# Kernel tuning notes

Hardware: AMD Instinct MI355X
Metric: run time of the kernel (lower is better)

## Reference

```python
import jax, jax.numpy as jnp
import numpy as np

FIELDS, NUM, CAT = 39, 13, 26
D, M, V, B, DEEP = 16, 16, 100000, 4096, 400
LEFT, RIGHT = np.triu_indices(FIELDS, k=1)  # pair indices, Q = 741
Q = LEFT.size
EPS = 1e-5


def setup_inputs() -> dict:
    key = jax.random.key(0)
    ks = jax.random.split(key, 18)
    xi = jax.random.randint(ks[0], (B, CAT), 0, V)
    xv = jax.random.uniform(ks[1], (B, NUM), dtype=jnp.float32)
    # 2nd-order embedding tables, stacked since all fields share vocab size
    emb_tables = jax.random.normal(ks[2], (FIELDS, V, D), dtype=jnp.float32) * 0.1
    T3 = jax.random.normal(ks[3], (D, M, D), dtype=jnp.float32) * 0.05
    T2 = jax.random.normal(ks[4], (M, D * D), dtype=jnp.float32) * 0.05
    gc = jax.random.normal(ks[5], (Q,), dtype=jnp.float32)
    fi_w = jax.random.normal(ks[6], (Q * M, DEEP), dtype=jnp.float32) * 0.01
    fi_b = jnp.zeros((DEEP,), dtype=jnp.float32)
    fi_gamma = jnp.ones((DEEP,), dtype=jnp.float32)
    fi_beta = jnp.zeros((DEEP,), dtype=jnp.float32)
    emb_w = jax.random.normal(ks[7], (FIELDS * D, DEEP), dtype=jnp.float32) * 0.02
    emb_b = jnp.zeros((DEEP,), dtype=jnp.float32)
    emb_gamma = jnp.ones((DEEP,), dtype=jnp.float32)
    emb_beta = jnp.zeros((DEEP,), dtype=jnp.float32)
    fc_w = jax.random.normal(ks[8], (2 * DEEP, 1), dtype=jnp.float32) * 0.05
    fc_b = jnp.zeros((1,), dtype=jnp.float32)
    return {"xi": xi, "xv": xv, "emb_tables": emb_tables, "T3": T3, "T2": T2,
            "gc": gc, "fi_w": fi_w, "fi_b": fi_b, "fi_gamma": fi_gamma, "fi_beta": fi_beta,
            "emb_w": emb_w, "emb_b": emb_b, "emb_gamma": emb_gamma, "emb_beta": emb_beta,
            "fc_w": fc_w, "fc_b": fc_b}


def _bn(x, gamma, beta):
    # BatchNorm1d in training mode: batch statistics, biased variance
    mean = jnp.mean(x, axis=0)
    var = jnp.var(x, axis=0)
    return gamma * (x - mean) * jax.lax.rsqrt(var + EPS) + beta


def reference(xi, xv, emb_tables, T3, T2, gc, fi_w, fi_b, fi_gamma, fi_beta,
              emb_w, emb_b, emb_gamma, emb_beta, fc_w, fc_b):
    # numerical fields: embedding row 0 scaled by the raw value
    num_part = xv[:, :, None] * emb_tables[:NUM, 0, :][None]          # [B, 13, D]
    # categorical fields: per-field gather
    cat_part = emb_tables[NUM + jnp.arange(CAT)[None, :], xi]          # [B, 26, D]
    fm2 = jnp.concatenate([num_part, cat_part], axis=1)               # [B, 39, D]
    vi = fm2[:, LEFT]                                                  # [B, Q, D]
    vj = fm2[:, RIGHT]                                                 # [B, Q, D]
    # einsum('bqd,dmd,bqd->bm'): repeated d on T3 takes its diagonal -> [D, M]
    T3diag = jnp.einsum('dmd->dm', T3)
    ga = jnp.einsum('bqd,bqd,dm->bm', vi, vj, T3diag)                  # [B, M]
    ga = jax.nn.softmax(ga, axis=1)
    # T1 = einsum('bm,mn->bmn'); s = einsum('bqd,bmn,bqd->bqm') sums T1 over n
    t1_rowsum = ga * jnp.sum(T2, axis=1)[None, :]                      # [B, M]
    pair_dot = jnp.einsum('bqd,bqd->bq', vi, vj)                       # [B, Q]
    s = pair_dot[:, :, None] * t1_rowsum[:, None, :]                   # [B, Q, M]
    sh = (s * gc[None, :, None]).reshape(-1, Q * M)                    # [B, Q*M]
    th = jax.nn.relu(_bn(sh @ fi_w + fi_b, fi_gamma, fi_beta))         # [B, DEEP]
    emb = fm2.reshape(-1, FIELDS * D)                                  # [B, 39*D]
    emb = jax.nn.relu(_bn(emb @ emb_w + emb_b, emb_gamma, emb_beta))   # [B, DEEP]
    out = jnp.concatenate([th, emb], axis=1) @ fc_w + fc_b             # [B, 1]
    return jnp.sum(jax.nn.sigmoid(out), axis=1)                        # [B]
```

## Files before the change

### kernel.cpp

```cpp
#include <hip/hip_runtime.h>
#include <hip/hip_bf16.h>

#define BATCH 4096
#define FIELDS_ 39
#define NUMF 13
#define CATF 26
#define DD 16
#define MM 16
#define VV 100000
#define DEEP_ 400
#define QQ 741
#define QPAD 768
#define KE 624
#define KEP 640
#define NEP 512
#define N1 6400
#define NKTE 20
#define NT_ 24
#define EPS_ 1e-5f

#define OFF_ABF 0
#define OFF_T   (BATCH*QPAD/2)
#define OFF_W2  (OFF_T + BATCH*MM)
#define OFF_WE  (OFF_W2 + N1*QPAD/2)
#define OFF_FMB (OFF_WE + NEP*KEP/2)
#define OFF_TH  (OFF_FMB + BATCH*KEP/2)
#define OFF_EMB (OFF_TH + BATCH*DEEP_)
#define OFF_ACC (OFF_EMB + BATCH*DEEP_)
#define OFF_T2S (OFF_ACC + 1600)
#define OFF_T3D (OFF_T2S + 16)
#define OFF_QIJ (OFF_T3D + 256)

typedef __attribute__((ext_vector_type(8))) short bf16x8;
typedef __attribute__((ext_vector_type(4))) float f32x4;

__device__ __forceinline__ ushort f2bf(float v) {
    union { float f; unsigned u; } x; x.f = v;
    unsigned r = x.u + 0x7fff + ((x.u >> 16) & 1);
    return (ushort)(r >> 16);
}
__device__ __forceinline__ unsigned pack2(float a, float b) {
    return (unsigned)f2bf(a) | ((unsigned)f2bf(b) << 16);
}
__device__ __forceinline__ void async16(void* lds, const void* g) {
    __builtin_amdgcn_global_load_lds(
        (const __attribute__((address_space(1))) unsigned int*)g,
        (__attribute__((address_space(3))) unsigned int*)lds,
        16, 0, 0);
}

__global__ __launch_bounds__(256) void kprep_all(const float* __restrict__ T3,
                                                 const float* __restrict__ T2,
                                                 const float* __restrict__ fi_w,
                                                 const float* __restrict__ emb_w,
                                                 float* __restrict__ ws,
                                                 ushort* __restrict__ W2,
                                                 ushort* __restrict__ WE) {
    __shared__ float tile[32][401];
    int bid = blockIdx.x, tid = threadIdx.x;
    if (bid == 0) {
        if (tid < MM) {
            float s = 0.f;
            for (int j = 0; j < DD * DD; ++j) s += T2[tid * DD * DD + j];
            ws[OFF_T2S + tid] = s;
        }
        if (tid < DD * MM) {
            int d = tid >> 4, m = tid & 15;
            ws[OFF_T3D + tid] = T3[(d * MM + m) * DD + d];
        }
        for (int i = tid; i < 1600; i += 256) ws[OFF_ACC + i] = 0.f;
        int* qij = (int*)(ws + OFF_QIJ);
        for (int q = tid; q < QPAD; q += 256) {
            int v = 0;
            if (q < QQ) {
                int i = 0, qq = q, cnt = FIELDS_ - 1;
                while (qq >= cnt) { qq -= cnt; ++i; cnt = FIELDS_ - 1 - i; }
                v = (i << 8) | (i + 1 + qq);
            }
            qij[q] = v;
        }
    } else if (bid <= 384) {
        int kt = (bid - 1) >> 4, m = (bid - 1) & 15;
        for (int i = tid; i < 32 * 100; i += 256) {
            int ql = i / 100, c4 = i - ql * 100;
            int q = kt * 32 + ql;
            float4 v = make_float4(0.f, 0.f, 0.f, 0.f);
            if (q < QQ) v = *(const float4*)&fi_w[(q * MM + m) * DEEP_ + c4 * 4];
            tile[ql][c4 * 4 + 0] = v.x; tile[ql][c4 * 4 + 1] = v.y;
            tile[ql][c4 * 4 + 2] = v.z; tile[ql][c4 * 4 + 3] = v.w;
        }
        __syncthreads();
        for (int i = tid; i < 400 * 4; i += 256) {
            int kcol = i >> 2, cq = i & 3;
            unsigned r[4];
#pragma unroll
            for (int j = 0; j < 4; ++j)
                r[j] = pack2(tile[cq * 8 + 2 * j][kcol], tile[cq * 8 + 2 * j + 1][kcol]);
            *(uint4*)&W2[(long)(kcol * 16 + m) * QPAD + kt * 32 + cq * 8] =
                make_uint4(r[0], r[1], r[2], r[3]);
        }
    } else {
        int kt = bid - 385;
        for (int i = tid; i < 32 * 100; i += 256) {
            int kl = i / 100, c4 = i - kl * 100;
            int k = kt * 32 + kl;
            float4 v = make_float4(0.f, 0.f, 0.f, 0.f);
            if (k < KE) v = *(const float4*)&emb_w[k * DEEP_ + c4 * 4];
            tile[kl][c4 * 4 + 0] = v.x; tile[kl][c4 * 4 + 1] = v.y;
            tile[kl][c4 * 4 + 2] = v.z; tile[kl][c4 * 4 + 3] = v.w;
        }
        __syncthreads();
        for (int i = tid; i < 512 * 4; i += 256) {
            int n = i >> 2, cq = i & 3;
            uint4 o = make_uint4(0, 0, 0, 0);
            if (n < DEEP_) {
                unsigned r[4];
#pragma unroll
                for (int j = 0; j < 4; ++j)
                    r[j] = pack2(tile[cq * 8 + 2 * j][n], tile[cq * 8 + 2 * j + 1][n]);
                o = make_uint4(r[0], r[1], r[2], r[3]);
            }
            *(uint4*)&WE[(long)n * KEP + kt * 32 + cq * 8] = o;
        }
    }
}

__global__ __launch_bounds__(256) void kfeat(const int* __restrict__ xi,
                                             const float* __restrict__ xv,
                                             const float* __restrict__ emb,
                                             const float* __restrict__ gc,
                                             float* __restrict__ ws,
                                             ushort* __restrict__ Abf,
                                             ushort* __restrict__ FMB) {
    __shared__ float row[KE];
    __shared__ float hsh[DD];
    __shared__ float gash[MM];
    int b = blockIdx.x, tid = threadIdx.x;
    for (int e = tid; e < KE; e += 256) {
        int f = e >> 4, d = e & 15;
        float v;
        if (f < NUMF) {
            v = xv[b * NUMF + f] * emb[(long)f * VV * DD + d];
        } else {
            int c = f - NUMF;
            int idxv = xi[b * CATF + c];
            v = emb[((long)(NUMF + c) * VV + idxv) * DD + d];
        }
        row[e] = v;
    }
    __syncthreads();
    for (int e = tid; e < KEP; e += 256)
        FMB[(long)b * KEP + e] = (e < KE) ? f2bf(row[e]) : (ushort)0;
    if (tid < DD) {
        float s = 0.f, s2 = 0.f;
        for (int f = 0; f < FIELDS_; ++f) { float v = row[f * DD + tid]; s += v; s2 += v * v; }
        hsh[tid] = 0.5f * (s * s - s2);
    }
    __syncthreads();
    if (tid < MM) {
        float g = 0.f;
        for (int d = 0; d < DD; ++d) g += hsh[d] * ws[OFF_T3D + d * MM + tid];
        gash[tid] = g;
    }
    __syncthreads();
    if (tid < MM) {
        float mx = -1e30f;
        for (int m = 0; m < MM; ++m) mx = fmaxf(mx, gash[m]);
        float se = 0.f;
        for (int m = 0; m < MM; ++m) se += expf(gash[m] - mx);
        ws[OFF_T + b * MM + tid] = expf(gash[tid] - mx) / se * ws[OFF_T2S + tid];
    }
    const int* qij = (const int*)(ws + OFF_QIJ);
    for (int q = tid; q < QPAD; q += 256) {
        float av = 0.f;
        if (q < QQ) {
            int ij = qij[q];
            int i = ij >> 8, j = ij & 255;
            float dot = 0.f;
#pragma unroll
            for (int d = 0; d < DD; ++d) dot += row[i * DD + d] * row[j * DD + d];
            av = dot * gc[q];
        }
        Abf[(long)b * QPAD + q] = f2bf(av);
    }
}

__device__ __forceinline__ void pipeline(const ushort* As, const ushort* Bs0,
                                         const ushort* Bs1, ushort* lds0, ushort* lds1,
                                         int tid, int nt, int f1b, int f2b, int sw,
                                         f32x4 (*acc)[4]) {
#define STAGEP(L, T) { \
    async16((L) + tid * 8, As + (T) * 32); \
    async16((L) + 4096 + tid * 8, Bs0 + (T) * 32); \
    async16((L) + 8192 + tid * 8, Bs1 + (T) * 32); }
    STAGEP(lds0, 0);
    asm volatile("s_waitcnt vmcnt(0)" ::: "memory");
    __builtin_amdgcn_s_barrier();
    for (int t = 0; t < nt; ++t) {
        __builtin_amdgcn_sched_barrier(0);
        ushort* cur = (t & 1) ? lds1 : lds0;
        ushort* nxt = (t & 1) ? lds0 : lds1;
        bf16x8 f1[4], f2[4];
#pragma unroll
        for (int r = 0; r < 4; ++r) f1[r] = *(const bf16x8*)&cur[f1b + r * 512 + sw];
#pragma unroll
        for (int c = 0; c < 4; ++c) f2[c] = *(const bf16x8*)&cur[f2b + c * 512 + sw];
        if (t + 1 < nt) STAGEP(nxt, t + 1);
        __builtin_amdgcn_s_setprio(1);
#pragma unroll
        for (int r = 0; r < 4; ++r)
#pragma unroll
            for (int c = 0; c < 4; ++c)
                acc[r][c] = __builtin_amdgcn_mfma_f32_16x16x32_bf16(f1[r], f2[c], acc[r][c], 0, 0, 0);
        __builtin_amdgcn_s_setprio(0);
        if (t + 1 < nt) { asm volatile("s_waitcnt vmcnt(0)" ::: "memory"); }
        __builtin_amdgcn_s_barrier();
    }
#undef STAGEP
}

__global__ __launch_bounds__(512, 4) void kgemms(const ushort* __restrict__ Abf,
                                                 const ushort* __restrict__ W2,
                                                 const ushort* __restrict__ FMB,
                                                 const ushort* __restrict__ WE,
                                                 const float* __restrict__ Tmat,
                                                 float* __restrict__ TH,
                                                 float* __restrict__ EMB,
                                                 float* __restrict__ ACC) {
    __shared__ ushort lds0[12288];
    __shared__ ushort lds1[12288];
    __shared__ float red[512];
    int tid = threadIdx.x;
    int lane = tid & 63, wid = tid >> 6;
    int wb = wid >> 2, wn = wid & 3;
    int kq = lane >> 4, lr = lane & 15;
    int arow = tid >> 2, ac = tid & 3;
    int csw = (ac ^ ((arow >> 1) & 3)) * 8;
    int sw = (kq ^ ((lr >> 1) & 3)) * 8;
    red[tid < 512 ? tid : 0] = 0.f;
    f32x4 acc[4][4] = {};
    int wg = blockIdx.x;

    if (wg < 800) {
        int s = (wg & 7) * 100 + (wg >> 3);
        int n0 = (s >> 5) * 256, b0 = (s & 31) * 128;
        const ushort* As  = Abf + (long)(b0 + arow) * QPAD + csw;
        const ushort* Bs0 = W2 + (long)(n0 + arow) * QPAD + csw;
        const ushort* Bs1 = W2 + (long)(n0 + 128 + arow) * QPAD + csw;
        pipeline(As, Bs0, Bs1, lds0, lds1, tid, NT_,
                 4096 + (wn * 64 + lr) * 32, (wb * 64 + lr) * 32, sw, acc);
        float ls[4] = {0.f, 0.f, 0.f, 0.f}, ls2[4] = {0.f, 0.f, 0.f, 0.f};
#pragma unroll
        for (int cg = 0; cg < 4; ++cg) {
            int bloc = wb * 64 + cg * 16 + lr;
            float4 t4 = *(const float4*)&Tmat[(b0 + bloc) * 16 + kq * 4];
#pragma unroll
            for (int r = 0; r < 4; ++r) {
                float v = acc[r][cg][0] * t4.x + acc[r][cg][1] * t4.y +
                          acc[r][cg][2] * t4.z + acc[r][cg][3] * t4.w;
                v += __shfl_xor(v, 16);
                v += __shfl_xor(v, 32);
                ls[r] += v; ls2[r] += v * v;
                if (lane < 16)
                    TH[(b0 + bloc) * DEEP_ + (n0 >> 4) + wn * 4 + r] = v;
            }
        }
#pragma unroll
        for (int r = 0; r < 4; ++r) {
            float a = ls[r], b2 = ls2[r];
            a += __shfl_xor(a, 8, 16); b2 += __shfl_xor(b2, 8, 16);
            a += __shfl_xor(a, 4, 16); b2 += __shfl_xor(b2, 4, 16);
            a += __shfl_xor(a, 2, 16); b2 += __shfl_xor(b2, 2, 16);
            a += __shfl_xor(a, 1, 16); b2 += __shfl_xor(b2, 1, 16);
            if (lane == 0) {
                atomicAdd(&red[wn * 4 + r], a);
                atomicAdd(&red[16 + wn * 4 + r], b2);
            }
        }
        __syncthreads();
        if (tid < 16) {
            atomicAdd(&ACC[(n0 >> 4) + tid], red[tid]);
            atomicAdd(&ACC[800 + (n0 >> 4) + tid], red[16 + tid]);
        }
    } else {
        int e = wg - 800;
        int se = (e & 7) * 8 + (e >> 3);
        int n0 = (se >> 5) * 256, b0 = (se & 31) * 128;
        const ushort* As  = FMB + (long)(b0 + arow) * KEP + csw;
        const ushort* Bs0 = WE + (long)(n0 + arow) * KEP + csw;
        const ushort* Bs1 = WE + (long)(n0 + 128 + arow) * KEP + csw;
        pipeline(As, Bs0, Bs1, lds0, lds1, tid, NKTE,
                 (wb * 64 + lr) * 32, 4096 + (wn * 64 + lr) * 32, sw, acc);
#pragma unroll
        for (int cg = 0; cg < 4; ++cg) {
            int ncl = wn * 64 + cg * 16 + lr;
            int nc = n0 + ncl;
            float ls = 0.f, ls2 = 0.f;
#pragma unroll
            for (int r = 0; r < 4; ++r) {
#pragma unroll
                for (int j = 0; j < 4; ++j) {
                    float v = acc[r][cg][j];
                    int brow = b0 + wb * 64 + r * 16 + kq * 4 + j;
                    if (nc < DEEP_) EMB[brow * DEEP_ + nc] = v;
                    ls += v; ls2 += v * v;
                }
            }
            ls += __shfl_xor(ls, 16);  ls += __shfl_xor(ls, 32);
            ls2 += __shfl_xor(ls2, 16); ls2 += __shfl_xor(ls2, 32);
            if (lane < 16 && nc < DEEP_) {
                atomicAdd(&red[ncl], ls);
                atomicAdd(&red[256 + ncl], ls2);
            }
        }
        __syncthreads();
        if (tid < 256) {
            int nc = n0 + tid;
            if (nc < DEEP_) {
                atomicAdd(&ACC[400 + nc], red[tid]);
                atomicAdd(&ACC[1200 + nc], red[256 + tid]);
            }
        }
    }
}

__global__ __launch_bounds__(256) void kfinal(const float* fig, const float* fibeta,
                                              const float* eg, const float* ebeta,
                                              const float* fcw, const float* fcb,
                                              const float* ws, float* out) {
    int b = blockIdx.x, tid = threadIdx.x;
    float part = 0.f;
    for (int c = tid; c < 800; c += 256) {
        float x, g, be;
        if (c < DEEP_) { x = ws[OFF_TH + b * DEEP_ + c]; g = fig[c]; be = fibeta[c]; }
        else { int cc = c - DEEP_; x = ws[OFF_EMB + b * DEEP_ + cc]; g = eg[cc]; be = ebeta[cc]; }
        float sm = ws[OFF_ACC + c], sq = ws[OFF_ACC + 800 + c];
        float mean = sm * (1.f / BATCH);
        float var = sq * (1.f / BATCH) - mean * mean;
        float rstd = rsqrtf(var + EPS_);
        float v = fmaxf(g * (x - mean) * rstd + be, 0.f);
        part += v * fcw[c];
    }
    __shared__ float red[4];
#pragma unroll
    for (int off = 32; off > 0; off >>= 1) part += __shfl_down(part, off, 64);
    if ((tid & 63) == 0) red[tid >> 6] = part;
    __syncthreads();
    if (tid == 0) {
        float tot = red[0] + red[1] + red[2] + red[3] + fcb[0];
        out[b] = 1.f / (1.f + expf(-tot));
    }
}

extern "C" void kernel_launch(void* const* d_in, const int* in_sizes, int n_in,
                              void* d_out, int out_size, void* d_ws, size_t ws_size,
                              hipStream_t stream) {
    const int*   xi    = (const int*)d_in[0];
    const float* xv    = (const float*)d_in[1];
    const float* emb   = (const float*)d_in[2];
    const float* T3    = (const float*)d_in[3];
    const float* T2    = (const float*)d_in[4];
    const float* gc    = (const float*)d_in[5];
    const float* fi_w  = (const float*)d_in[6];
    const float* fig   = (const float*)d_in[8];
    const float* fibt  = (const float*)d_in[9];
    const float* emb_w = (const float*)d_in[10];
    const float* eg    = (const float*)d_in[12];
    const float* ebt   = (const float*)d_in[13];
    const float* fcw   = (const float*)d_in[14];
    const float* fcb   = (const float*)d_in[15];
    float* ws = (float*)d_ws;
    ushort* Abf = (ushort*)(ws + OFF_ABF);
    ushort* W2  = (ushort*)(ws + OFF_W2);
    ushort* WE  = (ushort*)(ws + OFF_WE);
    ushort* FMB = (ushort*)(ws + OFF_FMB);
    float* out = (float*)d_out;

    hipLaunchKernelGGL(kprep_all, dim3(405), dim3(256), 0, stream,
                       T3, T2, fi_w, emb_w, ws, W2, WE);
    hipLaunchKernelGGL(kfeat, dim3(BATCH), dim3(256), 0, stream, xi, xv, emb, gc, ws, Abf, FMB);
    hipLaunchKernelGGL(kgemms, dim3(864), dim3(512), 0, stream,
                       Abf, W2, FMB, WE, ws + OFF_T, ws + OFF_TH, ws + OFF_EMB, ws + OFF_ACC);
    hipLaunchKernelGGL(kfinal, dim3(BATCH), dim3(256), 0, stream,
                       fig, fibt, eg, ebt, fcw, fcb, ws, out);
}
```

Before: 92.58 us.

## Fuse feature and weight-prep kernels, triple-buffer GEMM pipeline, vectorize stores

Splits the weight transpose/bf16 conversion into finer blocks and merges it with the per-sample feature kernel into one launch, so the two independent jobs overlap. The feature path now stages its bf16 outputs in shared memory and writes them with wide stores. It also computes the pair indices inline instead of reading a precomputed table. The GEMM pipeline goes from double to triple buffering with a prefetch distance of two and skips the final barrier. TH results are staged in LDS for float4 stores, and kfinal uses float4 loads. The triple buffer raises LDS use per block, which may reduce occupancy.

```diff
diff --git a/kernel.cpp b/kernel.cpp
--- a/kernel.cpp
+++ b/kernel.cpp
@@ -29,7 +29,6 @@
 #define OFF_ACC (OFF_EMB + BATCH*DEEP_)
 #define OFF_T2S (OFF_ACC + 1600)
 #define OFF_T3D (OFF_T2S + 16)
-#define OFF_QIJ (OFF_T3D + 256)
 
 typedef __attribute__((ext_vector_type(8))) short bf16x8;
 typedef __attribute__((ext_vector_type(4))) float f32x4;
@@ -49,163 +48,172 @@
         16, 0, 0);
 }
 
-__global__ __launch_bounds__(256) void kprep_all(const float* __restrict__ T3,
-                                                 const float* __restrict__ T2,
-                                                 const float* __restrict__ fi_w,
-                                                 const float* __restrict__ emb_w,
-                                                 float* __restrict__ ws,
-                                                 ushort* __restrict__ W2,
-                                                 ushort* __restrict__ WE) {
-    __shared__ float tile[32][401];
+__global__ __launch_bounds__(256) void kprep0(const float* __restrict__ T3,
+                                              const float* __restrict__ T2,
+                                              float* __restrict__ ws) {
+    int tid = threadIdx.x;
+    if (tid < MM) {
+        float s = 0.f;
+        for (int j = 0; j < DD * DD; ++j) s += T2[tid * DD * DD + j];
+        ws[OFF_T2S + tid] = s;
+    }
+    if (tid < DD * MM) {
+        int d = tid >> 4, m = tid & 15;
+        ws[OFF_T3D + tid] = T3[(d * MM + m) * DD + d];
+    }
+    for (int i = tid; i < 1600; i += 256) ws[OFF_ACC + i] = 0.f;
+}
+
+__global__ __launch_bounds__(256) void kbig(const int* __restrict__ xi,
+                                            const float* __restrict__ xv,
+                                            const float* __restrict__ emb,
+                                            const float* __restrict__ gc,
+                                            const float* __restrict__ fi_w,
+                                            const float* __restrict__ emb_w,
+                                            float* __restrict__ ws,
+                                            ushort* __restrict__ Abf,
+                                            ushort* __restrict__ FMB,
+                                            ushort* __restrict__ W2,
+                                            ushort* __restrict__ WE) {
+    __shared__ float smem[4200];
     int bid = blockIdx.x, tid = threadIdx.x;
-    if (bid == 0) {
+
+    if (bid < BATCH) {
+        float* row = smem;
+        float* hsh = smem + 624;
+        float* gash = smem + 640;
+        ushort* stA = (ushort*)(smem + 656);
+        ushort* stF = stA + QPAD;
+        int b = bid;
+        for (int e = tid; e < KE; e += 256) {
+            int f = e >> 4, d = e & 15;
+            float v;
+            if (f < NUMF) {
+                v = xv[b * NUMF + f] * emb[(long)f * VV * DD + d];
+            } else {
+                int c = f - NUMF;
+                int idxv = xi[b * CATF + c];
+                v = emb[((long)(NUMF + c) * VV + idxv) * DD + d];
+            }
+            row[e] = v;
+        }
+        __syncthreads();
+        for (int e = tid; e < KEP; e += 256)
+            stF[e] = (e < KE) ? f2bf(row[e]) : (ushort)0;
+        if (tid < DD) {
+            float s = 0.f, s2 = 0.f;
+            for (int f = 0; f < FIELDS_; ++f) { float v = row[f * DD + tid]; s += v; s2 += v * v; }
+            hsh[tid] = 0.5f * (s * s - s2);
+        }
+        __syncthreads();
         if (tid < MM) {
-            float s = 0.f;
-            for (int j = 0; j < DD * DD; ++j) s += T2[tid * DD * DD + j];
-            ws[OFF_T2S + tid] = s;
-        }
-        if (tid < DD * MM) {
-            int d = tid >> 4, m = tid & 15;
-            ws[OFF_T3D + tid] = T3[(d * MM + m) * DD + d];
-        }
-        for (int i = tid; i < 1600; i += 256) ws[OFF_ACC + i] = 0.f;
-        int* qij = (int*)(ws + OFF_QIJ);
+            float g = 0.f;
+            for (int d = 0; d < DD; ++d) g += hsh[d] * ws[OFF_T3D + d * MM + tid];
+            gash[tid] = g;
+        }
+        __syncthreads();
+        if (tid < MM) {
+            float mx = -1e30f;
+            for (int m = 0; m < MM; ++m) mx = fmaxf(mx, gash[m]);
+            float se = 0.f;
+            for (int m = 0; m < MM; ++m) se += expf(gash[m] - mx);
+            ws[OFF_T + b * MM + tid] = expf(gash[tid] - mx) / se * ws[OFF_T2S + tid];
+        }
         for (int q = tid; q < QPAD; q += 256) {
-            int v = 0;
+            float av = 0.f;
             if (q < QQ) {
                 int i = 0, qq = q, cnt = FIELDS_ - 1;
                 while (qq >= cnt) { qq -= cnt; ++i; cnt = FIELDS_ - 1 - i; }
-                v = (i << 8) | (i + 1 + qq);
-            }
-            qij[q] = v;
-        }
-    } else if (bid <= 384) {
-        int kt = (bid - 1) >> 4, m = (bid - 1) & 15;
-        for (int i = tid; i < 32 * 100; i += 256) {
-            int ql = i / 100, c4 = i - ql * 100;
+                int j = i + 1 + qq;
+                float dot = 0.f;
+#pragma unroll
+                for (int d = 0; d < DD; ++d) dot += row[i * DD + d] * row[j * DD + d];
+                av = dot * gc[q];
+            }
+            stA[q] = f2bf(av);
+        }
+        __syncthreads();
+        if (tid < 96)
+            *(uint4*)&Abf[(long)b * QPAD + tid * 8] = *(uint4*)&stA[tid * 8];
+        else if (tid < 176)
+            *(uint4*)&FMB[(long)b * KEP + (tid - 96) * 8] = *(uint4*)&stF[(tid - 96) * 8];
+    } else if (bid < BATCH + 1536) {
+        int bt = bid - BATCH;
+        int kt = bt >> 6, m = (bt >> 2) & 15, ch = bt & 3;
+        float* tile = smem;
+        for (int i = tid; i < 32 * 25; i += 256) {
+            int ql = i / 25, c4 = i - ql * 25;
             int q = kt * 32 + ql;
             float4 v = make_float4(0.f, 0.f, 0.f, 0.f);
-            if (q < QQ) v = *(const float4*)&fi_w[(q * MM + m) * DEEP_ + c4 * 4];
-            tile[ql][c4 * 4 + 0] = v.x; tile[ql][c4 * 4 + 1] = v.y;
-            tile[ql][c4 * 4 + 2] = v.z; tile[ql][c4 * 4 + 3] = v.w;
-        }
-        __syncthreads();
-        for (int i = tid; i < 400 * 4; i += 256) {
-            int kcol = i >> 2, cq = i & 3;
+            if (q < QQ) v = *(const float4*)&fi_w[(q * MM + m) * DEEP_ + ch * 100 + c4 * 4];
+            tile[ql * 101 + c4 * 4 + 0] = v.x; tile[ql * 101 + c4 * 4 + 1] = v.y;
+            tile[ql * 101 + c4 * 4 + 2] = v.z; tile[ql * 101 + c4 * 4 + 3] = v.w;
+        }
+        __syncthreads();
+        for (int i = tid; i < 100 * 4; i += 256) {
+            int lc = i >> 2, cq = i & 3;
+            int kcol = ch * 100 + lc;
             unsigned r[4];
 #pragma unroll
             for (int j = 0; j < 4; ++j)
-                r[j] = pack2(tile[cq * 8 + 2 * j][kcol], tile[cq * 8 + 2 * j + 1][kcol]);
+                r[j] = pack2(tile[(cq * 8 + 2 * j) * 101 + lc], tile[(cq * 8 + 2 * j + 1) * 101 + lc]);
             *(uint4*)&W2[(long)(kcol * 16 + m) * QPAD + kt * 32 + cq * 8] =
                 make_uint4(r[0], r[1], r[2], r[3]);
         }
     } else {
-        int kt = bid - 385;
-        for (int i = tid; i < 32 * 100; i += 256) {
-            int kl = i / 100, c4 = i - kl * 100;
+        int bt = bid - BATCH - 1536;
+        int kt = bt >> 2, ch = bt & 3;
+        float* tile = smem;
+        for (int i = tid; i < 32 * 32; i += 256) {
+            int kl = i >> 5, c4 = i & 31;
             int k = kt * 32 + kl;
+            int n = ch * 128 + c4 * 4;
             float4 v = make_float4(0.f, 0.f, 0.f, 0.f);
-            if (k < KE) v = *(const float4*)&emb_w[k * DEEP_ + c4 * 4];
-            tile[kl][c4 * 4 + 0] = v.x; tile[kl][c4 * 4 + 1] = v.y;
-            tile[kl][c4 * 4 + 2] = v.z; tile[kl][c4 * 4 + 3] = v.w;
-        }
-        __syncthreads();
-        for (int i = tid; i < 512 * 4; i += 256) {
-            int n = i >> 2, cq = i & 3;
+            if (k < KE && n < DEEP_) v = *(const float4*)&emb_w[k * DEEP_ + n];
+            tile[kl * 129 + c4 * 4 + 0] = v.x; tile[kl * 129 + c4 * 4 + 1] = v.y;
+            tile[kl * 129 + c4 * 4 + 2] = v.z; tile[kl * 129 + c4 * 4 + 3] = v.w;
+        }
+        __syncthreads();
+        for (int i = tid; i < 128 * 4; i += 256) {
+            int nl = i >> 2, cq = i & 3;
+            int n = ch * 128 + nl;
             uint4 o = make_uint4(0, 0, 0, 0);
             if (n < DEEP_) {
                 unsigned r[4];
 #pragma unroll
                 for (int j = 0; j < 4; ++j)
-                    r[j] = pack2(tile[cq * 8 + 2 * j][n], tile[cq * 8 + 2 * j + 1][n]);
+                    r[j] = pack2(tile[(cq * 8 + 2 * j) * 129 + nl], tile[(cq * 8 + 2 * j + 1) * 129 + nl]);
                 o = make_uint4(r[0], r[1], r[2], r[3]);
             }
-            *(uint4*)&WE[(long)n * KEP + kt * 32 + cq * 8] = o;
-        }
-    }
-}
-
-__global__ __launch_bounds__(256) void kfeat(const int* __restrict__ xi,
-                                             const float* __restrict__ xv,
-                                             const float* __restrict__ emb,
-                                             const float* __restrict__ gc,
-                                             float* __restrict__ ws,
-                                             ushort* __restrict__ Abf,
-                                             ushort* __restrict__ FMB) {
-    __shared__ float row[KE];
-    __shared__ float hsh[DD];
-    __shared__ float gash[MM];
-    int b = blockIdx.x, tid = threadIdx.x;
-    for (int e = tid; e < KE; e += 256) {
-        int f = e >> 4, d = e & 15;
-        float v;
-        if (f < NUMF) {
-            v = xv[b * NUMF + f] * emb[(long)f * VV * DD + d];
-        } else {
-            int c = f - NUMF;
-            int idxv = xi[b * CATF + c];
-            v = emb[((long)(NUMF + c) * VV + idxv) * DD + d];
-        }
-        row[e] = v;
-    }
-    __syncthreads();
-    for (int e = tid; e < KEP; e += 256)
-        FMB[(long)b * KEP + e] = (e < KE) ? f2bf(row[e]) : (ushort)0;
-    if (tid < DD) {
-        float s = 0.f, s2 = 0.f;
-        for (int f = 0; f < FIELDS_; ++f) { float v = row[f * DD + tid]; s += v; s2 += v * v; }
-        hsh[tid] = 0.5f * (s * s - s2);
-    }
-    __syncthreads();
-    if (tid < MM) {
-        float g = 0.f;
-        for (int d = 0; d < DD; ++d) g += hsh[d] * ws[OFF_T3D + d * MM + tid];
-        gash[tid] = g;
-    }
-    __syncthreads();
-    if (tid < MM) {
-        float mx = -1e30f;
-        for (int m = 0; m < MM; ++m) mx = fmaxf(mx, gash[m]);
-        float se = 0.f;
-        for (int m = 0; m < MM; ++m) se += expf(gash[m] - mx);
-        ws[OFF_T + b * MM + tid] = expf(gash[tid] - mx) / se * ws[OFF_T2S + tid];
-    }
-    const int* qij = (const int*)(ws + OFF_QIJ);
-    for (int q = tid; q < QPAD; q += 256) {
-        float av = 0.f;
-        if (q < QQ) {
-            int ij = qij[q];
-            int i = ij >> 8, j = ij & 255;
-            float dot = 0.f;
-#pragma unroll
-            for (int d = 0; d < DD; ++d) dot += row[i * DD + d] * row[j * DD + d];
-            av = dot * gc[q];
-        }
-        Abf[(long)b * QPAD + q] = f2bf(av);
-    }
-}
-
-__device__ __forceinline__ void pipeline(const ushort* As, const ushort* Bs0,
-                                         const ushort* Bs1, ushort* lds0, ushort* lds1,
-                                         int tid, int nt, int f1b, int f2b, int sw,
-                                         f32x4 (*acc)[4]) {
-#define STAGEP(L, T) { \
-    async16((L) + tid * 8, As + (T) * 32); \
-    async16((L) + 4096 + tid * 8, Bs0 + (T) * 32); \
-    async16((L) + 8192 + tid * 8, Bs1 + (T) * 32); }
-    STAGEP(lds0, 0);
-    asm volatile("s_waitcnt vmcnt(0)" ::: "memory");
+            if (n < NEP)
+                *(uint4*)&WE[(long)n * KEP + kt * 32 + cq * 8] = o;
+        }
+    }
+}
+
+__device__ __forceinline__ void pipeline3(const ushort* As, const ushort* Bs0,
+                                          const ushort* Bs1, ushort* lds,
+                                          int tid, int nt, int f1b, int f2b, int sw,
+                                          f32x4 (*acc)[4]) {
+#define STAGEP(SL, T) { \
+    ushort* L_ = lds + (SL) * 12288; \
+    async16(L_ + tid * 8, As + (T) * 32); \
+    async16(L_ + 4096 + tid * 8, Bs0 + (T) * 32); \
+    async16(L_ + 8192 + tid * 8, Bs1 + (T) * 32); }
+    STAGEP(0, 0); STAGEP(1, 1);
+    asm volatile("s_waitcnt vmcnt(3)" ::: "memory");
     __builtin_amdgcn_s_barrier();
+    int sl = 0;
     for (int t = 0; t < nt; ++t) {
         __builtin_amdgcn_sched_barrier(0);
-        ushort* cur = (t & 1) ? lds1 : lds0;
-        ushort* nxt = (t & 1) ? lds0 : lds1;
+        const ushort* cur = lds + sl * 12288;
         bf16x8 f1[4], f2[4];
 #pragma unroll
         for (int r = 0; r < 4; ++r) f1[r] = *(const bf16x8*)&cur[f1b + r * 512 + sw];
 #pragma unroll
         for (int c = 0; c < 4; ++c) f2[c] = *(const bf16x8*)&cur[f2b + c * 512 + sw];
-        if (t + 1 < nt) STAGEP(nxt, t + 1);
+        int sl2 = sl + 2; if (sl2 >= 3) sl2 -= 3;
+        if (t + 2 < nt) STAGEP(sl2, t + 2);
         __builtin_amdgcn_s_setprio(1);
 #pragma unroll
         for (int r = 0; r < 4; ++r)
@@ -213,8 +221,12 @@
             for (int c = 0; c < 4; ++c)
                 acc[r][c] = __builtin_amdgcn_mfma_f32_16x16x32_bf16(f1[r], f2[c], acc[r][c], 0, 0, 0);
         __builtin_amdgcn_s_setprio(0);
-        if (t + 1 < nt) { asm volatile("s_waitcnt vmcnt(0)" ::: "memory"); }
-        __builtin_amdgcn_s_barrier();
+        if (t + 1 < nt) {
+            if (t + 2 < nt) { asm volatile("s_waitcnt vmcnt(3)" ::: "memory"); }
+            else            { asm volatile("s_waitcnt vmcnt(0)" ::: "memory"); }
+            __builtin_amdgcn_s_barrier();
+        }
+        sl = sl + 1; if (sl >= 3) sl -= 3;
     }
 #undef STAGEP
 }
@@ -227,8 +239,7 @@
                                                  float* __restrict__ TH,
                                                  float* __restrict__ EMB,
                                                  float* __restrict__ ACC) {
-    __shared__ ushort lds0[12288];
-    __shared__ ushort lds1[12288];
+    __shared__ ushort ldsbuf[3 * 12288];
     __shared__ float red[512];
     int tid = threadIdx.x;
     int lane = tid & 63, wid = tid >> 6;
@@ -237,7 +248,7 @@
     int arow = tid >> 2, ac = tid & 3;
     int csw = (ac ^ ((arow >> 1) & 3)) * 8;
     int sw = (kq ^ ((lr >> 1) & 3)) * 8;
-    red[tid < 512 ? tid : 0] = 0.f;
+    red[tid] = 0.f;
     f32x4 acc[4][4] = {};
     int wg = blockIdx.x;
 
@@ -247,8 +258,9 @@
         const ushort* As  = Abf + (long)(b0 + arow) * QPAD + csw;
         const ushort* Bs0 = W2 + (long)(n0 + arow) * QPAD + csw;
         const ushort* Bs1 = W2 + (long)(n0 + 128 + arow) * QPAD + csw;
-        pipeline(As, Bs0, Bs1, lds0, lds1, tid, NT_,
-                 4096 + (wn * 64 + lr) * 32, (wb * 64 + lr) * 32, sw, acc);
+        pipeline3(As, Bs0, Bs1, ldsbuf, tid, NT_,
+                  4096 + (wn * 64 + lr) * 32, (wb * 64 + lr) * 32, sw, acc);
+        float* tbuf = (float*)ldsbuf;
         float ls[4] = {0.f, 0.f, 0.f, 0.f}, ls2[4] = {0.f, 0.f, 0.f, 0.f};
 #pragma unroll
         for (int cg = 0; cg < 4; ++cg) {
@@ -261,8 +273,7 @@
                 v += __shfl_xor(v, 16);
                 v += __shfl_xor(v, 32);
                 ls[r] += v; ls2[r] += v * v;
-                if (lane < 16)
-                    TH[(b0 + bloc) * DEEP_ + (n0 >> 4) + wn * 4 + r] = v;
+                if (kq == r) tbuf[bloc * 17 + wn * 4 + r] = v;
             }
         }
 #pragma unroll
@@ -282,6 +293,15 @@
             atomicAdd(&ACC[(n0 >> 4) + tid], red[tid]);
             atomicAdd(&ACC[800 + (n0 >> 4) + tid], red[16 + tid]);
         }
+        {
+            int rowl = tid >> 2, qf = tid & 3;
+            float o0 = tbuf[rowl * 17 + qf * 4 + 0];
+            float o1 = tbuf[rowl * 17 + qf * 4 + 1];
+            float o2 = tbuf[rowl * 17 + qf * 4 + 2];
+            float o3 = tbuf[rowl * 17 + qf * 4 + 3];
+            *(float4*)&TH[(b0 + rowl) * DEEP_ + (n0 >> 4) + qf * 4] =
+                make_float4(o0, o1, o2, o3);
+        }
     } else {
         int e = wg - 800;
         int se = (e & 7) * 8 + (e >> 3);
@@ -289,8 +309,8 @@
         const ushort* As  = FMB + (long)(b0 + arow) * KEP + csw;
         const ushort* Bs0 = WE + (long)(n0 + arow) * KEP + csw;
         const ushort* Bs1 = WE + (long)(n0 + 128 + arow) * KEP + csw;
-        pipeline(As, Bs0, Bs1, lds0, lds1, tid, NKTE,
-                 (wb * 64 + lr) * 32, 4096 + (wn * 64 + lr) * 32, sw, acc);
+        pipeline3(As, Bs0, Bs1, ldsbuf, tid, NKTE,
+                  (wb * 64 + lr) * 32, 4096 + (wn * 64 + lr) * 32, sw, acc);
 #pragma unroll
         for (int cg = 0; cg < 4; ++cg) {
             int ncl = wn * 64 + cg * 16 + lr;
@@ -324,22 +344,38 @@
     }
 }
 
-__global__ __launch_bounds__(256) void kfinal(const float* fig, const float* fibeta,
-                                              const float* eg, const float* ebeta,
-                                              const float* fcw, const float* fcb,
-                                              const float* ws, float* out) {
+__global__ __launch_bounds__(256) void kfinal(const float* __restrict__ fig,
+                                              const float* __restrict__ fibeta,
+                                              const float* __restrict__ eg,
+                                              const float* __restrict__ ebeta,
+                                              const float* __restrict__ fcw,
+                                              const float* __restrict__ fcb,
+                                              const float* __restrict__ ws,
+                                              float* __restrict__ out) {
     int b = blockIdx.x, tid = threadIdx.x;
     float part = 0.f;
-    for (int c = tid; c < 800; c += 256) {
-        float x, g, be;
-        if (c < DEEP_) { x = ws[OFF_TH + b * DEEP_ + c]; g = fig[c]; be = fibeta[c]; }
-        else { int cc = c - DEEP_; x = ws[OFF_EMB + b * DEEP_ + cc]; g = eg[cc]; be = ebeta[cc]; }
-        float sm = ws[OFF_ACC + c], sq = ws[OFF_ACC + 800 + c];
-        float mean = sm * (1.f / BATCH);
-        float var = sq * (1.f / BATCH) - mean * mean;
-        float rstd = rsqrtf(var + EPS_);
-        float v = fmaxf(g * (x - mean) * rstd + be, 0.f);
-        part += v * fcw[c];
+    if (tid < 200) {
+        int c = tid * 4;
+        int loc = (c < DEEP_) ? c : c - DEEP_;
+        const float* xp = (c < DEEP_) ? &ws[OFF_TH + b * DEEP_ + loc]
+                                      : &ws[OFF_EMB + b * DEEP_ + loc];
+        float4 x = *(const float4*)xp;
+        float4 g = *(const float4*)((c < DEEP_) ? &fig[loc] : &eg[loc]);
+        float4 be = *(const float4*)((c < DEEP_) ? &fibeta[loc] : &ebeta[loc]);
+        float4 sm = *(const float4*)&ws[OFF_ACC + c];
+        float4 sq = *(const float4*)&ws[OFF_ACC + 800 + c];
+        float4 w = *(const float4*)&fcw[c];
+        const float* xv_ = (const float*)&x; const float* gv = (const float*)&g;
+        const float* bev = (const float*)&be; const float* smv = (const float*)&sm;
+        const float* sqv = (const float*)&sq; const float* wv = (const float*)&w;
+#pragma unroll
+        for (int j = 0; j < 4; ++j) {
+            float mean = smv[j] * (1.f / BATCH);
+            float var = sqv[j] * (1.f / BATCH) - mean * mean;
+            float rstd = rsqrtf(var + EPS_);
+            float v = fmaxf(gv[j] * (xv_[j] - mean) * rstd + bev[j], 0.f);
+            part += v * wv[j];
+        }
     }
     __shared__ float red[4];
 #pragma unroll
@@ -376,9 +412,9 @@
     ushort* FMB = (ushort*)(ws + OFF_FMB);
     float* out = (float*)d_out;
 
-    hipLaunchKernelGGL(kprep_all, dim3(405), dim3(256), 0, stream,
-                       T3, T2, fi_w, emb_w, ws, W2, WE);
-    hipLaunchKernelGGL(kfeat, dim3(BATCH), dim3(256), 0, stream, xi, xv, emb, gc, ws, Abf, FMB);
+    hipLaunchKernelGGL(kprep0, dim3(1), dim3(256), 0, stream, T3, T2, ws);
+    hipLaunchKernelGGL(kbig, dim3(BATCH + 1536 + 80), dim3(256), 0, stream,
+                       xi, xv, emb, gc, fi_w, emb_w, ws, Abf, FMB, W2, WE);
     hipLaunchKernelGGL(kgemms, dim3(864), dim3(512), 0, stream,
                        Abf, W2, FMB, WE, ws + OFF_T, ws + OFF_TH, ws + OFF_EMB, ws + OFF_ACC);
     hipLaunchKernelGGL(kfinal, dim3(BATCH), dim3(256), 0, stream,
```

Result: no change. 91.49 us (-1.2%).
